# Kernel optimization log

Measured on AMD Instinct MI355X. Metric: run time of the kernel, lower is better.

## Reference

```python
import jax, jax.numpy as jnp
import numpy as np

T, B, MAXN = 16, 8, 256
N = B * MAXN            # flat node dim per timestep
IN_DIM, HID, OUT = 2, 64, 32
DENSITY = 0.01          # ~20 neighbors/node at N=2048


def setup_inputs() -> dict:
    key = jax.random.key(0)
    ks = jax.random.split(key, 14)
    x = jax.random.normal(ks[0], (T, N, IN_DIM), jnp.float32)
    adj = (jax.random.uniform(ks[1], (T, N, N)) < DENSITY).astype(jnp.float32)
    ego = jax.random.randint(ks[2], (B, T, MAXN), 0, 2).astype(bool)
    def glorot(k, shape):
        fan_in, fan_out = shape[0], shape[-1]
        s = jnp.sqrt(6.0 / (fan_in + fan_out))
        return jax.random.uniform(k, shape, jnp.float32, -s, s)
    W1 = glorot(ks[3], (IN_DIM, HID)); b1 = jnp.zeros((HID,), jnp.float32)
    W2 = glorot(ks[4], (HID, HID));    b2 = jnp.zeros((HID,), jnp.float32)
    su = 1.0 / jnp.sqrt(OUT)
    W_ih = jax.random.uniform(ks[5], (4 * OUT, HID), jnp.float32, -su, su)
    W_hh = jax.random.uniform(ks[6], (4 * OUT, OUT), jnp.float32, -su, su)
    b_ih = jax.random.uniform(ks[7], (4 * OUT,), jnp.float32, -su, su)
    b_hh = jax.random.uniform(ks[8], (4 * OUT,), jnp.float32, -su, su)
    Wa = jax.random.uniform(ks[9], (OUT,), jnp.float32, -su, su)
    ba = jnp.zeros((), jnp.float32)
    return dict(big_batch_positions=x, big_batched_adjacency_pruned=adj,
                ego_mask_batch=ego, W1=W1, b1=b1, W2=W2, b2=b2,
                W_ih=W_ih, W_hh=W_hh, b_ih=b_ih, b_hh=b_hh, Wa=Wa, ba=ba)


def _gcn(A_hat, x, W, b):
    # PyG GCNConv with self-loops already in A_hat: out[d] = d_d^-1/2 * sum_s A_hat[s,d] d_s^-1/2 (xW)[s] + b
    deg = A_hat.sum(axis=0)                       # [N] (column/dst degree incl. self-loop)
    dinv = jnp.where(deg > 0, jax.lax.rsqrt(deg), 0.0)
    xw = x @ W                                    # [N, out]
    return (A_hat.T @ (dinv[:, None] * xw)) * dinv[:, None] + b


def _forward(x, adj, ego, W1, b1, W2, b2, W_ih, W_hh, b_ih, b_hh, Wa, ba):
    Bb, Tt, Mn = ego.shape
    m = jnp.transpose(ego, (1, 0, 2)).reshape(Tt, -1)       # [T, N] bool
    mf = m.astype(x.dtype)
    # masked adjacency + self-loops on masked nodes (dense equivalent of the
    # original boolean-index / nonzero / edge_index subgraph construction)
    A_hat = adj * mf[:, :, None] * mf[:, None, :] + jax.vmap(jnp.diag)(mf)

    def per_t(A_t, x_t):
        h1 = jax.nn.relu(_gcn(A_t, x_t, W1, b1))
        return _gcn(A_t, h1, W2, b2)

    h2 = jax.vmap(per_t)(A_hat, x) * mf[..., None]          # [T, N, HID] (zeros off-mask)

    # faithful to original: nn.LSTM(batch_first=False) receives [N, T, HID],
    # i.e. sequence axis = nodes, batch axis = timesteps
    seq = jnp.transpose(h2, (1, 0, 2))                       # [N, T, HID]
    out_dim = W_hh.shape[1]
    h0 = jnp.zeros((Tt, out_dim), x.dtype)

    def step(carry, x_t):
        h, c = carry
        g = x_t @ W_ih.T + b_ih + h @ W_hh.T + b_hh          # [T, 4*OUT]
        i, f, gg, o = jnp.split(g, 4, axis=-1)
        c = jax.nn.sigmoid(f) * c + jax.nn.sigmoid(i) * jnp.tanh(gg)
        h = jax.nn.sigmoid(o) * jnp.tanh(c)
        return (h, c), h

    _, lstm_out = jax.lax.scan(step, (h0, h0), seq)          # [N, T, OUT]
    attn = jax.nn.softmax(lstm_out @ Wa + ba, axis=1)        # [N, T]
    pooled = jnp.einsum('ntd,nt->nd', lstm_out, attn)        # [N, OUT]
    return pooled.reshape(Bb, Mn, out_dim)


def reference(big_batch_positions, big_batched_adjacency_pruned, ego_mask_batch,
              W1, b1, W2, b2, W_ih, W_hh, b_ih, b_hh, Wa, ba):
    return _forward(big_batch_positions, big_batched_adjacency_pruned,
                    ego_mask_batch, W1, b1, W2, b2, W_ih, W_hh, b_ih, b_hh, Wa, ba)
```

## Files before the change

### kernel.cpp

```cpp
#include <hip/hip_runtime.h>
#include <stdint.h>

#define T_    16
#define N_    2048
#define CAP_  96
#define CHUNK_ 64
#define WARM_  192

typedef float v4 __attribute__((ext_vector_type(4)));
typedef float f32x4 __attribute__((ext_vector_type(4)));
typedef _Float16 f16x8 __attribute__((ext_vector_type(8)));

__device__ inline float frcp(float x){
#if __has_builtin(__builtin_amdgcn_rcpf)
  return __builtin_amdgcn_rcpf(x);
#else
  return 1.0f / x;
#endif
}
__device__ inline float fsig(float x){ return frcp(1.0f + __expf(-x)); }

__global__ __launch_bounds__(256) void k_mask(const uint8_t* __restrict__ ego_raw,
                                              float* __restrict__ m,
                                              int* __restrict__ cnt){
  __shared__ int s_int01, s_f01;
  const int tid = threadIdx.x;
  if (tid == 0){ s_int01 = 1; s_f01 = 1; }
  __syncthreads();
  const uint32_t* w = (const uint32_t*)ego_raw;
  int int01 = 1, f01 = 1;
  for (int i = tid; i < 8192; i += 256){
    uint32_t v = w[i];
    int01 &= (v <= 1u);
    f01   &= (v == 0u) || (v == 0x3F800000u);
  }
  if (!int01) atomicAnd(&s_int01, 0);
  if (!f01)   atomicAnd(&s_f01, 0);
  __syncthreads();
  const int mode = s_int01 ? 0 : (s_f01 ? 1 : 2);
  const int base = blockIdx.x * 2048;
  for (int q = tid; q < 2048; q += 256){
    int i = base + q;
    int t = i >> 11, n = i & 2047, b = n >> 8, j = n & 255;
    int src = (b*T_ + t)*256 + j;
    float val;
    if (mode == 0)      val = (((const int32_t*)ego_raw)[src] != 0)   ? 1.f : 0.f;
    else if (mode == 1) val = (((const float*)ego_raw)[src]  != 0.f)  ? 1.f : 0.f;
    else                val = (ego_raw[src] != 0)                     ? 1.f : 0.f;
    m[i] = val;
    cnt[i] = 0;
  }
}

__global__ __launch_bounds__(256) void k_sparsify(const float* __restrict__ adj,
                                                  const float* __restrict__ m,
                                                  int* __restrict__ cnt,
                                                  uint16_t* __restrict__ idx){
  const int bx = blockIdx.x;
  const int t  = bx >> 7;
  const int sg = bx & 127;
  const int tid = threadIdx.x;
  const int lane = tid & 63;
  const int tcol = t << 11;
  const float4* base4 = (const float4*)(adj + ((size_t)t << 22));
  const int d0a = tid << 2;
  const int d0b = (256 + tid) << 2;
  const float4 ma = *(const float4*)(m + tcol + d0a);
  const float4 mb = *(const float4*)(m + tcol + d0b);
  float mrow = (lane < 16) ? m[tcol + (sg << 4) + lane] : 0.f;
  const unsigned long long live = __ballot(mrow != 0.f) & 0xFFFFull;
  for (int sr = 0; sr < 16; sr++){
    if (!((live >> sr) & 1ull)) continue;
    int s = (sg << 4) + sr;
    const float4* row4 = base4 + ((size_t)s << 9);
    float4 va = row4[tid];
    float4 vb = row4[256 + tid];
    if (va.x != 0.f && ma.x != 0.f){ int p = atomicAdd(&cnt[tcol+d0a  ],1); if (p<CAP_) idx[(size_t)(tcol+d0a  )*CAP_+p]=(uint16_t)s; }
    if (va.y != 0.f && ma.y != 0.f){ int p = atomicAdd(&cnt[tcol+d0a+1],1); if (p<CAP_) idx[(size_t)(tcol+d0a+1)*CAP_+p]=(uint16_t)s; }
    if (va.z != 0.f && ma.z != 0.f){ int p = atomicAdd(&cnt[tcol+d0a+2],1); if (p<CAP_) idx[(size_t)(tcol+d0a+2)*CAP_+p]=(uint16_t)s; }
    if (va.w != 0.f && ma.w != 0.f){ int p = atomicAdd(&cnt[tcol+d0a+3],1); if (p<CAP_) idx[(size_t)(tcol+d0a+3)*CAP_+p]=(uint16_t)s; }
    if (vb.x != 0.f && mb.x != 0.f){ int p = atomicAdd(&cnt[tcol+d0b  ],1); if (p<CAP_) idx[(size_t)(tcol+d0b  )*CAP_+p]=(uint16_t)s; }
    if (vb.y != 0.f && mb.y != 0.f){ int p = atomicAdd(&cnt[tcol+d0b+1],1); if (p<CAP_) idx[(size_t)(tcol+d0b+1)*CAP_+p]=(uint16_t)s; }
    if (vb.z != 0.f && mb.z != 0.f){ int p = atomicAdd(&cnt[tcol+d0b+2],1); if (p<CAP_) idx[(size_t)(tcol+d0b+2)*CAP_+p]=(uint16_t)s; }
    if (vb.w != 0.f && mb.w != 0.f){ int p = atomicAdd(&cnt[tcol+d0b+3],1); if (p<CAP_) idx[(size_t)(tcol+d0b+3)*CAP_+p]=(uint16_t)s; }
  }
}

__global__ __launch_bounds__(64) void k_gcn1v2(const float* __restrict__ x,
                                               const float* __restrict__ W1,
                                               const float* __restrict__ b1,
                                               const float* __restrict__ W2,
                                               const int* __restrict__ cnt,
                                               const uint16_t* __restrict__ idx,
                                               const float* __restrict__ m,
                                               float* __restrict__ v2){
  __shared__ float h1s[64];
  const int col = blockIdx.x;
  const int lane = threadIdx.x;
  const float mcol = m[col];
  if (mcol <= 0.5f){
    v2[(size_t)col*64 + lane] = 0.f;
    return;
  }
  const int craw = cnt[col];
  int c = craw; if (c > CAP_) c = CAP_;
  const float dc = rsqrtf(1.0f + (float)craw);
  const int tbase = col & ~2047;
  const uint16_t* lst = idx + (size_t)col*CAP_;
  const float w1a = W1[lane], w1b = W1[64 + lane];
  const float2* x2 = (const float2*)x;
  float2 xs = x2[col];
  float acc = dc*(xs.x*w1a + xs.y*w1b);
  int i = 0;
  for (; i + 4 <= c; i += 4){
    ushort4 s4 = *(const ushort4*)(lst + i);
    int sa = tbase+s4.x, sb = tbase+s4.y, sc = tbase+s4.z, sd = tbase+s4.w;
    float da = rsqrtf(1.0f + (float)cnt[sa]);
    float db = rsqrtf(1.0f + (float)cnt[sb]);
    float dcc= rsqrtf(1.0f + (float)cnt[sc]);
    float dd = rsqrtf(1.0f + (float)cnt[sd]);
    float2 xa = x2[sa], xb = x2[sb], xc = x2[sc], xd = x2[sd];
    acc += da*(xa.x*w1a + xa.y*w1b) + db*(xb.x*w1a + xb.y*w1b)
         + dcc*(xc.x*w1a + xc.y*w1b) + dd*(xd.x*w1a + xd.y*w1b);
  }
  for (; i < c; i++){
    int s = tbase + lst[i];
    float ds = rsqrtf(1.0f + (float)cnt[s]);
    float2 xv = x2[s];
    acc += ds*(xv.x*w1a + xv.y*w1b);
  }
  float y = dc*acc + b1[lane];
  h1s[lane] = fmaxf(y, 0.f);
  __syncthreads();
  float s = 0.f;
  #pragma unroll 8
  for (int h = 0; h < 64; h++) s += h1s[h]*W2[h*64 + lane];
  v2[(size_t)col*64 + lane] = dc*s;
}

__global__ __launch_bounds__(64) void k_agg2pre(const float* __restrict__ v,
                                                const int* __restrict__ cnt,
                                                const uint16_t* __restrict__ idx,
                                                const float* __restrict__ m,
                                                const float* __restrict__ b2,
                                                const float* __restrict__ Wih,
                                                const float* __restrict__ bih,
                                                const float* __restrict__ bhh,
                                                float* __restrict__ P4){
  __shared__ float h2s[64];
  const int col = blockIdx.x;
  const int lane = threadIdx.x;
  const float mc = m[col];
  if (mc <= 0.5f){
    #pragma unroll
    for (int o = lane; o < 128; o += 64){
      const int j = o;
      const int dst = (j & 31)*4 + (j >> 5);
      P4[(size_t)col*128 + dst] = bih[j] + bhh[j];
    }
    return;
  }
  const int craw = cnt[col];
  int c = craw; if (c > CAP_) c = CAP_;
  const float dc = rsqrtf(1.0f + (float)craw);
  const int tbase = col & ~2047;
  const uint16_t* lst = idx + (size_t)col*CAP_;
  float acc = v[(size_t)col*64 + lane];
  int i = 0;
  for (; i + 4 <= c; i += 4){
    ushort4 s4 = *(const ushort4*)(lst + i);
    float a0 = v[((size_t)tbase + s4.x)*64 + lane];
    float a1 = v[((size_t)tbase + s4.y)*64 + lane];
    float a2 = v[((size_t)tbase + s4.z)*64 + lane];
    float a3 = v[((size_t)tbase + s4.w)*64 + lane];
    acc += (a0 + a1) + (a2 + a3);
  }
  for (; i < c; i++) acc += v[((size_t)tbase + lst[i])*64 + lane];
  h2s[lane] = dc*acc + b2[lane];
  __syncthreads();
  #pragma unroll
  for (int o = lane; o < 128; o += 64){
    const int j = o;
    const v4* hrow = (const v4*)h2s;
    const v4* wr = (const v4*)(Wih + j*64);
    float a0 = bih[j] + bhh[j], a1 = 0.f, a2 = 0.f, a3 = 0.f;
    #pragma unroll
    for (int q = 0; q < 16; q++){
      v4 hv = hrow[q], wv = wr[q];
      a0 = fmaf(wv.x, hv.x, a0);
      a1 = fmaf(wv.y, hv.y, a1);
      a2 = fmaf(wv.z, hv.z, a2);
      a3 = fmaf(wv.w, hv.w, a3);
    }
    const int dst = (j & 31)*4 + (j >> 5);
    P4[(size_t)col*128 + dst] = (a0 + a1) + (a2 + a3);
  }
}

__global__ __attribute__((amdgpu_flat_work_group_size(64,64), amdgpu_waves_per_eu(1,1)))
void k_lstm(const float* __restrict__ P4,
            const float* __restrict__ Whh,
            _Float16* __restrict__ L16){
  const int t   = blockIdx.x & 15;
  const int seg = blockIdx.x >> 4;
  const int l = threadIdx.x;
  const int c4 = l & 15, q = l >> 4;
  const int j = l & 31;
#define LB(B) f16x8 b##B; { const float* wr = Whh + (size_t)(16*B + c4)*32 + 8*q; \
    f16x8 tmp; tmp[0]=(_Float16)wr[0]; tmp[1]=(_Float16)wr[1]; tmp[2]=(_Float16)wr[2]; \
    tmp[3]=(_Float16)wr[3]; tmp[4]=(_Float16)wr[4]; tmp[5]=(_Float16)wr[5]; \
    tmp[6]=(_Float16)wr[6]; tmp[7]=(_Float16)wr[7]; b##B = tmp; } asm("" : "+v"(b##B));
  LB(0) LB(1) LB(2) LB(3) LB(4) LB(5) LB(6) LB(7)
#undef LB
  __shared__ __align__(16) _Float16 hs[64];
  hs[l] = (_Float16)0.f;
  const float4* Pt = (const float4*)P4 + (size_t)t*N_*32 + j;
  _Float16* Lt = L16 + (size_t)t*N_*64;
  float c = 0.f;
  const f32x4 zero = {0.f, 0.f, 0.f, 0.f};
  const bool hiq = (l & 16) != 0;

  const int ns   = seg*CHUNK_;
  int nw0 = ns - WARM_; if (nw0 < 0) nw0 = 0;
  const int nend = ns + CHUNK_;

  float4 p0 = Pt[(size_t)nw0*32], p1 = Pt[(size_t)(nw0+1)*32];

  auto step = [&](int n, bool prefetch, bool store) __attribute__((always_inline)) {
    float4 cur = p0; p0 = p1;
    if (prefetch) p1 = Pt[(size_t)(n + 2)*32];
    f16x8 af = *(const f16x8*)(hs + 8*q);
    f32x4 d0 = __builtin_amdgcn_mfma_f32_16x16x32_f16(af, b0, zero, 0, 0, 0);
    f32x4 d1 = __builtin_amdgcn_mfma_f32_16x16x32_f16(af, b1, zero, 0, 0, 0);
    f32x4 d2 = __builtin_amdgcn_mfma_f32_16x16x32_f16(af, b2, zero, 0, 0, 0);
    f32x4 d3 = __builtin_amdgcn_mfma_f32_16x16x32_f16(af, b3, zero, 0, 0, 0);
    f32x4 d4 = __builtin_amdgcn_mfma_f32_16x16x32_f16(af, b4, zero, 0, 0, 0);
    f32x4 d5 = __builtin_amdgcn_mfma_f32_16x16x32_f16(af, b5, zero, 0, 0, 0);
    f32x4 d6 = __builtin_amdgcn_mfma_f32_16x16x32_f16(af, b6, zero, 0, 0, 0);
    f32x4 d7 = __builtin_amdgcn_mfma_f32_16x16x32_f16(af, b7, zero, 0, 0, 0);
    float gi = cur.x + (hiq ? d1[0] : d0[0]);
    float gf = cur.y + (hiq ? d3[0] : d2[0]);
    float gg = cur.z + (hiq ? d5[0] : d4[0]);
    float go = cur.w + (hiq ? d7[0] : d6[0]);
    float iv = fsig(gi);
    float fv = fsig(gf);
    float gv = fmaf(2.0f, fsig(2.0f*gg), -1.0f);
    float ov = fsig(go);
    c = fmaf(fv, c, iv*gv);
    float th = fmaf(2.0f, fsig(2.0f*c), -1.0f);
    float hn = ov*th;
    _Float16 hf = (_Float16)hn;
    hs[l] = hf;
    if (store) Lt[n*64 + l] = hf;
  };

  int n = nw0;
  #pragma unroll 2
  for (; n < ns; n++) step(n, true, false);
  #pragma unroll 2
  for (; n < nend - 2; n++) step(n, true, true);
  step(nend - 2, false, true);
  step(nend - 1, false, true);
}

__global__ __launch_bounds__(256) void k_attn(const _Float16* __restrict__ L16,
                                              const float* __restrict__ Wa,
                                              float* __restrict__ out){
  __shared__ float sLDS[128];
  const int tid = threadIdx.x;
  const int sub = tid >> 5, k = tid & 31;
  const int n = blockIdx.x*8 + sub;
  if (k < 16){
    const int t = k;
    const f16x8* row = (const f16x8*)(L16 + ((size_t)(t << 11) + n)*64);
    const float4* wa4 = (const float4*)Wa;
    float s = 0.f;
    #pragma unroll
    for (int qq = 0; qq < 4; qq++){
      f16x8 hv = row[qq];
      float4 w0 = wa4[2*qq], w1 = wa4[2*qq+1];
      s += (float)hv[0]*w0.x + (float)hv[1]*w0.y + (float)hv[2]*w0.z + (float)hv[3]*w0.w
         + (float)hv[4]*w1.x + (float)hv[5]*w1.y + (float)hv[6]*w1.z + (float)hv[7]*w1.w;
    }
    sLDS[sub*16 + t] = s;
  }
  __syncthreads();
  float sc[16]; float mx = -1e30f;
  #pragma unroll
  for (int t = 0; t < 16; t++){ float v = sLDS[sub*16 + t]; sc[t] = v; mx = fmaxf(mx, v); }
  float sum = 0.f;
  #pragma unroll
  for (int t = 0; t < 16; t++){ float e = __expf(sc[t] - mx); sc[t] = e; sum += e; }
  const float inv = frcp(sum);
  float acc = 0.f;
  #pragma unroll
  for (int t = 0; t < 16; t++) acc += sc[t]*(float)L16[((size_t)(t << 11) + n)*64 + k];
  out[n*32 + k] = acc*inv;
}

extern "C" void kernel_launch(void* const* d_in, const int* in_sizes, int n_in,
                              void* d_out, int out_size, void* d_ws, size_t ws_size,
                              hipStream_t stream){
  (void)in_sizes; (void)n_in; (void)out_size; (void)ws_size;
  const float*   x   = (const float*)d_in[0];
  const float*   adj = (const float*)d_in[1];
  const uint8_t* ego = (const uint8_t*)d_in[2];
  const float*   W1  = (const float*)d_in[3];
  const float*   b1  = (const float*)d_in[4];
  const float*   W2  = (const float*)d_in[5];
  const float*   b2  = (const float*)d_in[6];
  const float*   Wih = (const float*)d_in[7];
  const float*   Whh = (const float*)d_in[8];
  const float*   bih = (const float*)d_in[9];
  const float*   bhh = (const float*)d_in[10];
  const float*   Wa  = (const float*)d_in[11];
  float* out = (float*)d_out;
  char* ws = (char*)d_ws;

  float*     m    = (float*)(ws);
  int*       cnt  = (int*)  (ws + 262144);
  uint16_t*  idx  = (uint16_t*)(ws + 393216);
  float*     v2   = (float*)(ws + 6684672);
  float*     P4   = (float*)(ws + 15073280);
  _Float16*  L16  = (_Float16*)v2;

  k_mask    <<<16,    256, 0, stream>>>(ego, m, cnt);
  k_sparsify<<<2048,  256, 0, stream>>>(adj, m, cnt, idx);
  k_gcn1v2  <<<32768, 64,  0, stream>>>(x, W1, b1, W2, cnt, idx, m, v2);
  k_agg2pre <<<32768, 64,  0, stream>>>(v2, cnt, idx, m, b2, Wih, bih, bhh, P4);
  k_lstm    <<<512,   64,  0, stream>>>(P4, Whh, L16);
  k_attn    <<<256,   256, 0, stream>>>(L16, Wa, out);
}
```

Measured before the change: 530.4 us.

## Parallelize GCN1 neighbor gather across lanes and double LSTM chunk count

```diff
diff --git a/kernel.cpp b/kernel.cpp
--- a/kernel.cpp
+++ b/kernel.cpp
@@ -4,7 +4,7 @@
 #define T_    16
 #define N_    2048
 #define CAP_  96
-#define CHUNK_ 64
+#define CHUNK_ 32
 #define WARM_  192
 
 typedef float v4 __attribute__((ext_vector_type(4)));
@@ -107,35 +107,42 @@
   const float dc = rsqrtf(1.0f + (float)craw);
   const int tbase = col & ~2047;
   const uint16_t* lst = idx + (size_t)col*CAP_;
-  const float w1a = W1[lane], w1b = W1[64 + lane];
   const float2* x2 = (const float2*)x;
-  float2 xs = x2[col];
-  float acc = dc*(xs.x*w1a + xs.y*w1b);
-  int i = 0;
-  for (; i + 4 <= c; i += 4){
-    ushort4 s4 = *(const ushort4*)(lst + i);
-    int sa = tbase+s4.x, sb = tbase+s4.y, sc = tbase+s4.z, sd = tbase+s4.w;
-    float da = rsqrtf(1.0f + (float)cnt[sa]);
-    float db = rsqrtf(1.0f + (float)cnt[sb]);
-    float dcc= rsqrtf(1.0f + (float)cnt[sc]);
-    float dd = rsqrtf(1.0f + (float)cnt[sd]);
-    float2 xa = x2[sa], xb = x2[sb], xc = x2[sc], xd = x2[sd];
-    acc += da*(xa.x*w1a + xa.y*w1b) + db*(xb.x*w1a + xb.y*w1b)
-         + dcc*(xc.x*w1a + xc.y*w1b) + dd*(xd.x*w1a + xd.y*w1b);
-  }
-  for (; i < c; i++){
-    int s = tbase + lst[i];
+  const float2 xs = x2[col];
+  float sx = 0.f, sy = 0.f;
+  if (lane < c){
+    int s = tbase + lst[lane];
     float ds = rsqrtf(1.0f + (float)cnt[s]);
     float2 xv = x2[s];
-    acc += ds*(xv.x*w1a + xv.y*w1b);
-  }
-  float y = dc*acc + b1[lane];
+    sx = ds*xv.x; sy = ds*xv.y;
+  }
+  if (lane + 64 < c){
+    int s = tbase + lst[lane + 64];
+    float ds = rsqrtf(1.0f + (float)cnt[s]);
+    float2 xv = x2[s];
+    sx += ds*xv.x; sy += ds*xv.y;
+  }
+  #pragma unroll
+  for (int off = 32; off; off >>= 1){
+    sx += __shfl_xor(sx, off, 64);
+    sy += __shfl_xor(sy, off, 64);
+  }
+  sx += dc*xs.x;
+  sy += dc*xs.y;
+  float y = dc*(sx*W1[lane] + sy*W1[64 + lane]) + b1[lane];
   h1s[lane] = fmaxf(y, 0.f);
   __syncthreads();
-  float s = 0.f;
-  #pragma unroll 8
-  for (int h = 0; h < 64; h++) s += h1s[h]*W2[h*64 + lane];
-  v2[(size_t)col*64 + lane] = dc*s;
+  const v4* h4 = (const v4*)h1s;
+  float a0 = 0.f, a1 = 0.f, a2 = 0.f, a3 = 0.f;
+  #pragma unroll
+  for (int qq = 0; qq < 16; qq++){
+    v4 hv = h4[qq];
+    a0 = fmaf(hv.x, W2[(4*qq + 0)*64 + lane], a0);
+    a1 = fmaf(hv.y, W2[(4*qq + 1)*64 + lane], a1);
+    a2 = fmaf(hv.z, W2[(4*qq + 2)*64 + lane], a2);
+    a3 = fmaf(hv.w, W2[(4*qq + 3)*64 + lane], a3);
+  }
+  v2[(size_t)col*64 + lane] = dc*((a0 + a1) + (a2 + a3));
 }
 
 __global__ __launch_bounds__(64) void k_agg2pre(const float* __restrict__ v,
@@ -328,6 +335,6 @@
   k_sparsify<<<2048,  256, 0, stream>>>(adj, m, cnt, idx);
   k_gcn1v2  <<<32768, 64,  0, stream>>>(x, W1, b1, W2, cnt, idx, m, v2);
   k_agg2pre <<<32768, 64,  0, stream>>>(v2, cnt, idx, m, b2, Wih, bih, bhh, P4);
-  k_lstm    <<<512,   64,  0, stream>>>(P4, Whh, L16);
+  k_lstm    <<<1024,  64,  0, stream>>>(P4, Whh, L16);
   k_attn    <<<256,   256, 0, stream>>>(L16, Wa, out);
 }
```

Result: faster. 518.4 us (-2.3%).
